# Kernel optimization log

Measured on AMD Instinct MI355X. Metric: run time of the kernel, lower is better.

The kernel has to match this reference:

```python
import jax, jax.numpy as jnp
import numpy as np
from jax import lax

B, C, H, W = 8, 128, 256, 256
OUT_CH = 64
IN_CH = C * 9  # 1152: module's in_channels = 9 * image channels (unfold with 3x3 kernel)


def setup_inputs() -> dict:
    key = jax.random.key(0)
    k1, k2, k3 = jax.random.split(key, 3)
    x = jax.random.normal(k1, (B, C, H, W), dtype=jnp.float32)
    style = jax.random.normal(k2, (B, IN_CH), dtype=jnp.float32)
    # learned parameter: torch.randn(out_channels, in_channels, 1, 1) -> store as (out, in)
    weight = jax.random.normal(k3, (OUT_CH, IN_CH), dtype=jnp.float32)
    return {"x": x, "style": style, "weight": weight}


def reference(x, style, weight):
    b, c, h, w = x.shape
    out_ch, in_ch = weight.shape  # in_ch == c * 9
    # unfold column ordering is (c, kh, kw), so the flattened weight is exactly a
    # 3x3 conv kernel: (out, c*9) -> (out, c, 3, 3)
    w33 = weight.reshape(out_ch, c, 3, 3)
    # style.view(B,1,in_ch,1,1) * weight -> per-sample modulated 3x3 kernels
    w_mod = style.reshape(b, 1, c, 3, 3) * w33[None]  # (B, out, c, 3, 3)

    def conv_one(xi, wi):
        # xi: (c, h, w), wi: (out, c, 3, 3); SAME padding matches padding=(1,1)
        return lax.conv_general_dilated(
            xi[None], wi, window_strides=(1, 1), padding="SAME",
            dimension_numbers=("NCHW", "OIHW", "NCHW"))[0]

    out = jax.vmap(conv_one)(x, w_mod)  # (B, out, h, w)
    return out
```

## Files before the change

### kernel.cpp

```cpp
#include <hip/hip_runtime.h>
#include <hip/hip_bf16.h>

#define BATCH 8
#define CIN   128
#define HH    256
#define WW    256
#define OUTC  64
#define INCH  1152
#define HW    (HH*WW)
#define WMOD_BYTES ((size_t)BATCH * 9 * OUTC * CIN * 2)

typedef __attribute__((ext_vector_type(8))) short short8;
typedef __attribute__((ext_vector_type(4))) float f32x4;
typedef __attribute__((ext_vector_type(4), aligned(4))) float f32x4u;

__device__ __forceinline__ unsigned short bf16r(float f) {
    unsigned u = __builtin_bit_cast(unsigned, f);
    u += 0x7fffu + ((u >> 16) & 1u);
    return (unsigned short)(u >> 16);
}

__global__ void __launch_bounds__(256) wmod_kernel(const float* __restrict__ weight,
                                                   const float* __restrict__ style,
                                                   unsigned short* __restrict__ wmod) {
    int i = blockIdx.x * 256 + threadIdx.x;
    if (i >= BATCH * 9 * OUTC * CIN) return;
    int c    = i & (CIN - 1);
    int rest = i >> 7;
    int o    = rest & (OUTC - 1);
    int bt   = rest >> 6;
    int tap  = bt % 9;
    int b    = bt / 9;
    int k    = c * 9 + tap;
    wmod[i] = bf16r(weight[o * INCH + k] * style[b * INCH + k]);
}

template <bool GW>
__global__ void __launch_bounds__(128, 2) conv4_kernel(
    const float* __restrict__ x,
    const unsigned short* __restrict__ wmod,
    const float* __restrict__ weight,
    const float* __restrict__ style,
    float* __restrict__ out)
{
    __shared__ __align__(16) unsigned short xs_sm[2][108 * 32];

    const int tid = threadIdx.x;
    const int bx  = blockIdx.x;
    const int b   = blockIdx.y;
    const int h0  = (bx >> 4) * 4;
    const int w0  = (bx & 15) * 16;

    const int wr  = tid >> 6;
    const int l15 = tid & 15;
    const int kg  = (tid >> 4) & 3;

    {
        short8 z = {0, 0, 0, 0, 0, 0, 0, 0};
        short8* p = (short8*)&xs_sm[0][0];
        for (int i = tid; i < 2 * 108 * 32 / 8; i += 128) p[i] = z;
    }

    const bool tval = tid < 120;
    const int tt  = tval ? tid : 0;
    const int cg  = tt / 30;
    const int rem = tt % 30;
    const int sr  = rem / 5;
    const int wq  = rem % 5;
    const int sh  = h0 - 1 + sr;
    const bool hok = tval && ((unsigned)sh < HH);
    const int wl  = w0 - 1 + wq * 4;
    const int wlc = min(max(wl, 0), WW - 4);
    const int colbase = wlc - (w0 - 1);
    const float* xsrc = x + ((size_t)(b * CIN + cg * 8)) * HW +
                        (hok ? sh : 0) * WW + wlc;

    f32x4 acc[2][4];
#pragma unroll
    for (int mi = 0; mi < 2; ++mi)
#pragma unroll
        for (int ni = 0; ni < 4; ++ni) acc[mi][ni] = (f32x4){0.f, 0.f, 0.f, 0.f};

    short8 A[9][2];
    f32x4  g[8];

    auto stageLoad = [&](int chunk) {
        if (hok) {
#pragma unroll
            for (int j = 0; j < 8; ++j)
                g[j] = *(const f32x4u*)(xsrc + (size_t)(chunk * 32 + j) * HW);
        }
    };

    auto stageWrite = [&](unsigned short* buf) {
        if (hok) {
#pragma unroll
            for (int u = 0; u < 4; ++u) {
                int col = colbase + u;
                if (col >= 0 && col <= 17) {
                    int s  = sr * 18 + col;
                    int gr = cg ^ (s & 3);
                    short8 sv;
#pragma unroll
                    for (int j = 0; j < 8; ++j) sv[j] = (short)bf16r(g[j][u]);
                    *(short8*)&buf[s * 32 + gr * 8] = sv;
                }
            }
        }
    };

    auto loadA = [&](int chunk) {
        if (GW) {
            const unsigned short* wb =
                wmod + ((size_t)(b * 9) * OUTC) * CIN + chunk * 32 + kg * 8;
#pragma unroll
            for (int tap = 0; tap < 9; ++tap)
#pragma unroll
                for (int mi = 0; mi < 2; ++mi)
                    A[tap][mi] = *(const short8*)(
                        wb + ((size_t)tap * OUTC + wr * 32 + mi * 16 + l15) * CIN);
        } else {
#pragma unroll
            for (int tap = 0; tap < 9; ++tap)
#pragma unroll
                for (int mi = 0; mi < 2; ++mi) {
                    int o = wr * 32 + mi * 16 + l15;
#pragma unroll
                    for (int j = 0; j < 8; ++j) {
                        int c = chunk * 32 + kg * 8 + j;
                        int k = c * 9 + tap;
                        A[tap][mi][j] = (short)bf16r(weight[o * INCH + k] *
                                                     style[b * INCH + k]);
                    }
                }
        }
    };

    auto compute = [&](const unsigned short* buf) {
#pragma unroll
        for (int kh = 0; kh < 3; ++kh)
#pragma unroll
            for (int kw = 0; kw < 3; ++kw) {
                const int tap = kh * 3 + kw;
                short8 Bv[4];
#pragma unroll
                for (int ni = 0; ni < 4; ++ni) {
                    int s  = (ni + kh) * 18 + (l15 + kw);
                    int gr = kg ^ (s & 3);
                    Bv[ni] = *(const short8*)&buf[s * 32 + gr * 8];
                }
#pragma unroll
                for (int mi = 0; mi < 2; ++mi)
#pragma unroll
                    for (int ni = 0; ni < 4; ++ni)
                        acc[mi][ni] = __builtin_amdgcn_mfma_f32_16x16x32_bf16(
                            A[tap][mi], Bv[ni], acc[mi][ni], 0, 0, 0);
            }
    };

    __syncthreads();

    stageLoad(0);
    loadA(0);
    stageWrite(xs_sm[0]);
    __syncthreads();

    stageLoad(1);
    __builtin_amdgcn_sched_barrier(0);
    compute(xs_sm[0]);
    __builtin_amdgcn_sched_barrier(0);
    loadA(1);
    stageWrite(xs_sm[1]);
    __syncthreads();

    stageLoad(2);
    __builtin_amdgcn_sched_barrier(0);
    compute(xs_sm[1]);
    __builtin_amdgcn_sched_barrier(0);
    loadA(2);
    stageWrite(xs_sm[0]);
    __syncthreads();

    stageLoad(3);
    __builtin_amdgcn_sched_barrier(0);
    compute(xs_sm[0]);
    __builtin_amdgcn_sched_barrier(0);
    loadA(3);
    stageWrite(xs_sm[1]);
    __syncthreads();

    compute(xs_sm[1]);

    float* op = out + ((size_t)b * OUTC) * HW + (size_t)h0 * WW + w0 + l15;
#pragma unroll
    for (int mi = 0; mi < 2; ++mi)
#pragma unroll
        for (int ni = 0; ni < 4; ++ni)
#pragma unroll
            for (int rr = 0; rr < 4; ++rr) {
                int o = wr * 32 + mi * 16 + kg * 4 + rr;
                op[(size_t)o * HW + ni * WW] = acc[mi][ni][rr];
            }
}

extern "C" void kernel_launch(void* const* d_in, const int* in_sizes, int n_in,
                              void* d_out, int out_size, void* d_ws, size_t ws_size,
                              hipStream_t stream) {
    const float* x      = (const float*)d_in[0];
    const float* style  = (const float*)d_in[1];
    const float* weight = (const float*)d_in[2];
    float* out = (float*)d_out;

    const int wmod_total = BATCH * 9 * OUTC * CIN;

    if (ws_size >= WMOD_BYTES) {
        unsigned short* wmodp = (unsigned short*)d_ws;
        wmod_kernel<<<(wmod_total + 255) / 256, 256, 0, stream>>>(weight, style, wmodp);
        conv4_kernel<true><<<dim3(1024, BATCH), 128, 0, stream>>>(
            x, wmodp, nullptr, nullptr, out);
    } else {
        conv4_kernel<false><<<dim3(1024, BATCH), 128, 0, stream>>>(
            x, nullptr, weight, style, out);
    }
}
```

Before: 264.3 us.

## Widen conv tile to 32 columns with 4 waves sharing staged input

The conv kernel now uses 256 threads covering a 4x32 output tile, with two wave-columns sharing one LDS input halo of 6x34 pixels. This raises input reuse per staged byte and halves the block count. The global loads become 16-byte aligned float4 loads. Out-of-bounds columns are now zero-filled explicitly, which replaces the upfront LDS zeroing. The XOR swizzle on LDS is removed, so bank conflicts may increase, and the larger block may lower occupancy.

```diff
diff --git a/kernel.cpp b/kernel.cpp
--- a/kernel.cpp
+++ b/kernel.cpp
@@ -12,7 +12,6 @@
 
 typedef __attribute__((ext_vector_type(8))) short short8;
 typedef __attribute__((ext_vector_type(4))) float f32x4;
-typedef __attribute__((ext_vector_type(4), aligned(4))) float f32x4u;
 
 __device__ __forceinline__ unsigned short bf16r(float f) {
     unsigned u = __builtin_bit_cast(unsigned, f);
@@ -36,74 +35,65 @@
 }
 
 template <bool GW>
-__global__ void __launch_bounds__(128, 2) conv4_kernel(
+__global__ void __launch_bounds__(256, 2) conv9_kernel(
     const float* __restrict__ x,
     const unsigned short* __restrict__ wmod,
     const float* __restrict__ weight,
     const float* __restrict__ style,
     float* __restrict__ out)
 {
-    __shared__ __align__(16) unsigned short xs_sm[2][108 * 32];
+    __shared__ __align__(16) unsigned short xs_sm[2][204 * 32];
 
     const int tid = threadIdx.x;
     const int bx  = blockIdx.x;
     const int b   = blockIdx.y;
-    const int h0  = (bx >> 4) * 4;
-    const int w0  = (bx & 15) * 16;
-
-    const int wr  = tid >> 6;
+    const int h0  = (bx >> 3) * 4;
+    const int w0  = (bx & 7) * 32;
+
+    const int wv  = tid >> 6;
+    const int wr  = wv >> 1;
+    const int wc  = wv & 1;
     const int l15 = tid & 15;
     const int kg  = (tid >> 4) & 3;
 
-    {
-        short8 z = {0, 0, 0, 0, 0, 0, 0, 0};
-        short8* p = (short8*)&xs_sm[0][0];
-        for (int i = tid; i < 2 * 108 * 32 / 8; i += 128) p[i] = z;
-    }
-
-    const bool tval = tid < 120;
-    const int tt  = tval ? tid : 0;
-    const int cg  = tt / 30;
-    const int rem = tt % 30;
-    const int sr  = rem / 5;
-    const int wq  = rem % 5;
+    const bool tv = tid < 240;
+    const int tt  = tv ? tid : 0;
+    const int cg  = tt / 60;
+    const int rem = tt % 60;
+    const int sr  = rem / 10;
+    const int qw  = rem % 10;
     const int sh  = h0 - 1 + sr;
-    const bool hok = tval && ((unsigned)sh < HH);
-    const int wl  = w0 - 1 + wq * 4;
+    const bool hok = tv && ((unsigned)sh < HH);
+    const int wl  = w0 - 4 + qw * 4;
     const int wlc = min(max(wl, 0), WW - 4);
-    const int colbase = wlc - (w0 - 1);
-    const float* xsrc = x + ((size_t)(b * CIN + cg * 8)) * HW +
-                        (hok ? sh : 0) * WW + wlc;
-
-    f32x4 acc[2][4];
-#pragma unroll
-    for (int mi = 0; mi < 2; ++mi)
-#pragma unroll
-        for (int ni = 0; ni < 4; ++ni) acc[mi][ni] = (f32x4){0.f, 0.f, 0.f, 0.f};
-
+    const int colbase = wl - (w0 - 1);
+    const float* xbase = x + ((size_t)(b * CIN + cg * 8)) * HW +
+                         (hok ? sh : 0) * WW + wlc;
+
+    f32x4  f[8];
     short8 A[9][2];
-    f32x4  g[8];
-
-    auto stageLoad = [&](int chunk) {
+
+    auto loadG = [&](int chunk) {
         if (hok) {
 #pragma unroll
             for (int j = 0; j < 8; ++j)
-                g[j] = *(const f32x4u*)(xsrc + (size_t)(chunk * 32 + j) * HW);
+                f[j] = *(const f32x4*)(xbase + (size_t)(chunk * 32 + j) * HW);
         }
     };
 
-    auto stageWrite = [&](unsigned short* buf) {
-        if (hok) {
+    auto writeG = [&](unsigned short* buf) {
+        if (tv) {
 #pragma unroll
             for (int u = 0; u < 4; ++u) {
                 int col = colbase + u;
-                if (col >= 0 && col <= 17) {
-                    int s  = sr * 18 + col;
-                    int gr = cg ^ (s & 3);
+                if (col >= 0 && col < 34) {
+                    bool wok = hok && ((unsigned)(wl + u) < WW);
                     short8 sv;
 #pragma unroll
-                    for (int j = 0; j < 8; ++j) sv[j] = (short)bf16r(g[j][u]);
-                    *(short8*)&buf[s * 32 + gr * 8] = sv;
+                    for (int j = 0; j < 8; ++j)
+                        sv[j] = wok ? (short)bf16r(f[j][u]) : (short)0;
+                    int s = sr * 34 + col;
+                    *(short8*)&buf[s * 32 + cg * 8] = sv;
                 }
             }
         }
@@ -136,6 +126,12 @@
         }
     };
 
+    f32x4 acc[2][4];
+#pragma unroll
+    for (int mi = 0; mi < 2; ++mi)
+#pragma unroll
+        for (int ni = 0; ni < 4; ++ni) acc[mi][ni] = (f32x4){0.f, 0.f, 0.f, 0.f};
+
     auto compute = [&](const unsigned short* buf) {
 #pragma unroll
         for (int kh = 0; kh < 3; ++kh)
@@ -145,9 +141,8 @@
                 short8 Bv[4];
 #pragma unroll
                 for (int ni = 0; ni < 4; ++ni) {
-                    int s  = (ni + kh) * 18 + (l15 + kw);
-                    int gr = kg ^ (s & 3);
-                    Bv[ni] = *(const short8*)&buf[s * 32 + gr * 8];
+                    int s = (ni + kh) * 34 + wc * 16 + l15 + kw;
+                    Bv[ni] = *(const short8*)&buf[s * 32 + kg * 8];
                 }
 #pragma unroll
                 for (int mi = 0; mi < 2; ++mi)
@@ -158,40 +153,39 @@
             }
     };
 
-    __syncthreads();
-
-    stageLoad(0);
+    loadG(0);
     loadA(0);
-    stageWrite(xs_sm[0]);
-    __syncthreads();
-
-    stageLoad(1);
+    __builtin_amdgcn_sched_barrier(0);
+    writeG(xs_sm[0]);
+    __syncthreads();
+
+    loadG(1);
     __builtin_amdgcn_sched_barrier(0);
     compute(xs_sm[0]);
     __builtin_amdgcn_sched_barrier(0);
     loadA(1);
-    stageWrite(xs_sm[1]);
-    __syncthreads();
-
-    stageLoad(2);
+    writeG(xs_sm[1]);
+    __syncthreads();
+
+    loadG(2);
     __builtin_amdgcn_sched_barrier(0);
     compute(xs_sm[1]);
     __builtin_amdgcn_sched_barrier(0);
     loadA(2);
-    stageWrite(xs_sm[0]);
-    __syncthreads();
-
-    stageLoad(3);
+    writeG(xs_sm[0]);
+    __syncthreads();
+
+    loadG(3);
     __builtin_amdgcn_sched_barrier(0);
     compute(xs_sm[0]);
     __builtin_amdgcn_sched_barrier(0);
     loadA(3);
-    stageWrite(xs_sm[1]);
+    writeG(xs_sm[1]);
     __syncthreads();
 
     compute(xs_sm[1]);
 
-    float* op = out + ((size_t)b * OUTC) * HW + (size_t)h0 * WW + w0 + l15;
+    float* op = out + ((size_t)b * OUTC) * HW + (size_t)h0 * WW + w0 + wc * 16 + l15;
 #pragma unroll
     for (int mi = 0; mi < 2; ++mi)
 #pragma unroll
@@ -216,10 +210,10 @@
     if (ws_size >= WMOD_BYTES) {
         unsigned short* wmodp = (unsigned short*)d_ws;
         wmod_kernel<<<(wmod_total + 255) / 256, 256, 0, stream>>>(weight, style, wmodp);
-        conv4_kernel<true><<<dim3(1024, BATCH), 128, 0, stream>>>(
+        conv9_kernel<true><<<dim3(512, BATCH), 256, 0, stream>>>(
             x, wmodp, nullptr, nullptr, out);
     } else {
-        conv4_kernel<false><<<dim3(1024, BATCH), 128, 0, stream>>>(
+        conv9_kernel<false><<<dim3(512, BATCH), 256, 0, stream>>>(
             x, nullptr, weight, style, out);
     }
 }
```

New measurement: 228.3 us. 1.16x faster.
